# Performance work log

Hardware: AMD Instinct MI355X
Metric: run time of the kernel (lower is better)

The kernel has to match this reference:

```python
import jax, jax.numpy as jnp
import numpy as np

N, M, D = 4096, 4096, 16


def setup_inputs() -> dict:
    key = jax.random.key(0)
    k1, k2, k3, k4 = jax.random.split(key, 4)
    x = jax.random.normal(k1, (N, D), dtype=jnp.float32)
    xx = jax.random.normal(k2, (M, D), dtype=jnp.float32)
    # free-form (pre-softplus) kernel parameters
    scale_ff = jax.random.uniform(k3, (D,), dtype=jnp.float32)
    variance_ff = jax.random.uniform(k4, (), dtype=jnp.float32)
    return {"x": x, "xx": xx, "scale_ff": scale_ff, "variance_ff": variance_ff}


def reference(x, xx, scale_ff, variance_ff):
    # positive() in AutoForce is softplus (free_form is its inverse)
    scale = jax.nn.softplus(scale_ff)          # [D]
    variance = jax.nn.softplus(variance_ff)    # scalar (diag amplitude)
    # r: [N, M, D] pairwise scaled differences (the large broadcast intermediate)
    r = (x[:, None, :] - xx[None, :, :]) / scale
    # K = exp(-||r||^2 / 2) * variance, shape [N, M]
    cov = jnp.exp(-0.5 * jnp.sum(r * r, axis=-1)) * variance
    return cov
```

## Files before the change

kernel.cpp:

```cpp
#include <hip/hip_runtime.h>
#include <math.h>


#define NN 4096
#define MM 4096
#define DD 16

__global__ __launch_bounds__(256, 4)
void rbf_kernel(const float* __restrict__ x, const float* __restrict__ xx,
                const float* __restrict__ scale_ff,
                const float* __restrict__ variance_ff,
                float* __restrict__ out) {
  __shared__ __align__(16) float s_inv[DD];
  __shared__ float s_var;
  __shared__ __align__(16) float s_x[64 * DD];

  const int tid  = threadIdx.x;
  const int lane = tid & 63;
  const int wave = tid >> 6;

  const int i0 = blockIdx.y * 64;
  const int j0 = blockIdx.x * 256;

  if (tid < DD) {
    s_inv[tid] = 1.0f / log1pf(expf(scale_ff[tid]));
  }
  if (tid == DD) {
    s_var = log1pf(expf(variance_ff[0]));
  }
  __syncthreads();

  {
    const int row = tid >> 2;
    const int c   = tid & 3;
    float4 xv = *(const float4*)&x[(i0 + row) * DD + c * 4];
    float4 iv = *(const float4*)&s_inv[c * 4];
    xv.x *= iv.x; xv.y *= iv.y; xv.z *= iv.z; xv.w *= iv.w;
    *(float4*)&s_x[row * DD + c * 4] = xv;
  }

  float4 b[4][4];
  {
    float4 iv[4];
#pragma unroll
    for (int c = 0; c < 4; ++c) iv[c] = *(const float4*)&s_inv[c * 4];
    const int jb = j0 + (lane << 2);
#pragma unroll
    for (int r = 0; r < 4; ++r) {
#pragma unroll
      for (int c = 0; c < 4; ++c) {
        float4 v = *(const float4*)&xx[(jb + r) * DD + c * 4];
        v.x *= iv[c].x; v.y *= iv[c].y; v.z *= iv[c].z; v.w *= iv[c].w;
        b[r][c] = v;
      }
    }
  }

  __syncthreads();

  const float var = s_var;
  const int jb = j0 + (lane << 2);

#pragma unroll
  for (int ii = 0; ii < 16; ++ii) {
    const int li = wave * 16 + ii;
    const float4* a4 = (const float4*)&s_x[li * DD];

    float acc0 = 0.f, acc1 = 0.f, acc2 = 0.f, acc3 = 0.f;
#pragma unroll
    for (int c = 0; c < 4; ++c) {
      const float4 a = a4[c];
      float d;
      d = a.x - b[0][c].x; acc0 = fmaf(d, d, acc0);
      d = a.y - b[0][c].y; acc0 = fmaf(d, d, acc0);
      d = a.z - b[0][c].z; acc0 = fmaf(d, d, acc0);
      d = a.w - b[0][c].w; acc0 = fmaf(d, d, acc0);

      d = a.x - b[1][c].x; acc1 = fmaf(d, d, acc1);
      d = a.y - b[1][c].y; acc1 = fmaf(d, d, acc1);
      d = a.z - b[1][c].z; acc1 = fmaf(d, d, acc1);
      d = a.w - b[1][c].w; acc1 = fmaf(d, d, acc1);

      d = a.x - b[2][c].x; acc2 = fmaf(d, d, acc2);
      d = a.y - b[2][c].y; acc2 = fmaf(d, d, acc2);
      d = a.z - b[2][c].z; acc2 = fmaf(d, d, acc2);
      d = a.w - b[2][c].w; acc2 = fmaf(d, d, acc2);

      d = a.x - b[3][c].x; acc3 = fmaf(d, d, acc3);
      d = a.y - b[3][c].y; acc3 = fmaf(d, d, acc3);
      d = a.z - b[3][c].z; acc3 = fmaf(d, d, acc3);
      d = a.w - b[3][c].w; acc3 = fmaf(d, d, acc3);
    }

    float4 o;
    o.x = __expf(-0.5f * acc0) * var;
    o.y = __expf(-0.5f * acc1) * var;
    o.z = __expf(-0.5f * acc2) * var;
    o.w = __expf(-0.5f * acc3) * var;
    *(float4*)&out[(size_t)(i0 + li) * MM + jb] = o;
  }
}

extern "C" void kernel_launch(void* const* d_in, const int* in_sizes, int n_in,
                              void* d_out, int out_size, void* d_ws, size_t ws_size,
                              hipStream_t stream) {
  const float* x   = (const float*)d_in[0];
  const float* xx  = (const float*)d_in[1];
  const float* sc  = (const float*)d_in[2];
  const float* var = (const float*)d_in[3];
  float* out = (float*)d_out;

  dim3 grid(MM / 256, NN / 64);
  dim3 block(256);
  rbf_kernel<<<grid, block, 0, stream>>>(x, xx, sc, var, out);
}
```

Measured before the change: 93.17 us.

## Expand squared distance into norms plus dot product, fold variance into exponent

Rewrites ||a-b||^2/2 as |a|^2/2 + |b|^2/2 - a·b, with per-row norms precomputed once (x norms in padded shared memory, xx norms in registers). The log of the variance is folded into the exponent, so the inner loop becomes pure FMAs and the per-output multiply disappears. The shared row stride is padded to 20 floats, and the row loop is unrolled by 2 instead of fully. The expansion can lose precision through cancellation for close points, and the kernel is probably bound by output store bandwidth anyway.

```diff
diff --git a/kernel.cpp b/kernel.cpp
--- a/kernel.cpp
+++ b/kernel.cpp
@@ -5,6 +5,7 @@
 #define NN 4096
 #define MM 4096
 #define DD 16
+#define RS 20
 
 __global__ __launch_bounds__(256, 4)
 void rbf_kernel(const float* __restrict__ x, const float* __restrict__ xx,
@@ -12,8 +13,8 @@
                 const float* __restrict__ variance_ff,
                 float* __restrict__ out) {
   __shared__ __align__(16) float s_inv[DD];
-  __shared__ float s_var;
-  __shared__ __align__(16) float s_x[64 * DD];
+  __shared__ float s_lnvar;
+  __shared__ __align__(16) float s_a[64 * RS];
 
   const int tid  = threadIdx.x;
   const int lane = tid & 63;
@@ -26,7 +27,7 @@
     s_inv[tid] = 1.0f / log1pf(expf(scale_ff[tid]));
   }
   if (tid == DD) {
-    s_var = log1pf(expf(variance_ff[0]));
+    s_lnvar = logf(log1pf(expf(variance_ff[0])));
   }
   __syncthreads();
 
@@ -36,10 +37,23 @@
     float4 xv = *(const float4*)&x[(i0 + row) * DD + c * 4];
     float4 iv = *(const float4*)&s_inv[c * 4];
     xv.x *= iv.x; xv.y *= iv.y; xv.z *= iv.z; xv.w *= iv.w;
-    *(float4*)&s_x[row * DD + c * 4] = xv;
+    *(float4*)&s_a[row * RS + c * 4] = xv;
+  }
+  __syncthreads();
+
+  if (tid < 64) {
+    float s = 0.f;
+#pragma unroll
+    for (int c = 0; c < 4; ++c) {
+      float4 v = *(const float4*)&s_a[tid * RS + c * 4];
+      s = fmaf(v.x, v.x, s); s = fmaf(v.y, v.y, s);
+      s = fmaf(v.z, v.z, s); s = fmaf(v.w, v.w, s);
+    }
+    s_a[tid * RS + DD] = 0.5f * s - s_lnvar;
   }
 
   float4 b[4][4];
+  float dn[4];
   {
     float4 iv[4];
 #pragma unroll
@@ -47,56 +61,53 @@
     const int jb = j0 + (lane << 2);
 #pragma unroll
     for (int r = 0; r < 4; ++r) {
+      float s = 0.f;
 #pragma unroll
       for (int c = 0; c < 4; ++c) {
-        float4 v = *(const float4*)&xx[(jb + r) * DD + c * 4];
+        float4 v = *(const float4*)&xx[(size_t)(jb + r) * DD + c * 4];
         v.x *= iv[c].x; v.y *= iv[c].y; v.z *= iv[c].z; v.w *= iv[c].w;
         b[r][c] = v;
+        s = fmaf(v.x, v.x, s); s = fmaf(v.y, v.y, s);
+        s = fmaf(v.z, v.z, s); s = fmaf(v.w, v.w, s);
       }
+      dn[r] = 0.5f * s;
     }
   }
 
   __syncthreads();
 
-  const float var = s_var;
   const int jb = j0 + (lane << 2);
 
-#pragma unroll
+#pragma unroll 2
   for (int ii = 0; ii < 16; ++ii) {
     const int li = wave * 16 + ii;
-    const float4* a4 = (const float4*)&s_x[li * DD];
+    const float* ap = &s_a[li * RS];
+    const float4 a0 = *(const float4*)&ap[0];
+    const float4 a1 = *(const float4*)&ap[4];
+    const float4 a2 = *(const float4*)&ap[8];
+    const float4 a3 = *(const float4*)&ap[12];
+    const float cc  = ap[DD];
 
-    float acc0 = 0.f, acc1 = 0.f, acc2 = 0.f, acc3 = 0.f;
+    float acc[4] = {0.f, 0.f, 0.f, 0.f};
 #pragma unroll
-    for (int c = 0; c < 4; ++c) {
-      const float4 a = a4[c];
-      float d;
-      d = a.x - b[0][c].x; acc0 = fmaf(d, d, acc0);
-      d = a.y - b[0][c].y; acc0 = fmaf(d, d, acc0);
-      d = a.z - b[0][c].z; acc0 = fmaf(d, d, acc0);
-      d = a.w - b[0][c].w; acc0 = fmaf(d, d, acc0);
-
-      d = a.x - b[1][c].x; acc1 = fmaf(d, d, acc1);
-      d = a.y - b[1][c].y; acc1 = fmaf(d, d, acc1);
-      d = a.z - b[1][c].z; acc1 = fmaf(d, d, acc1);
-      d = a.w - b[1][c].w; acc1 = fmaf(d, d, acc1);
-
-      d = a.x - b[2][c].x; acc2 = fmaf(d, d, acc2);
-      d = a.y - b[2][c].y; acc2 = fmaf(d, d, acc2);
-      d = a.z - b[2][c].z; acc2 = fmaf(d, d, acc2);
-      d = a.w - b[2][c].w; acc2 = fmaf(d, d, acc2);
-
-      d = a.x - b[3][c].x; acc3 = fmaf(d, d, acc3);
-      d = a.y - b[3][c].y; acc3 = fmaf(d, d, acc3);
-      d = a.z - b[3][c].z; acc3 = fmaf(d, d, acc3);
-      d = a.w - b[3][c].w; acc3 = fmaf(d, d, acc3);
+    for (int r = 0; r < 4; ++r) {
+      float s = 0.f;
+      s = fmaf(a0.x, b[r][0].x, s); s = fmaf(a0.y, b[r][0].y, s);
+      s = fmaf(a0.z, b[r][0].z, s); s = fmaf(a0.w, b[r][0].w, s);
+      s = fmaf(a1.x, b[r][1].x, s); s = fmaf(a1.y, b[r][1].y, s);
+      s = fmaf(a1.z, b[r][1].z, s); s = fmaf(a1.w, b[r][1].w, s);
+      s = fmaf(a2.x, b[r][2].x, s); s = fmaf(a2.y, b[r][2].y, s);
+      s = fmaf(a2.z, b[r][2].z, s); s = fmaf(a2.w, b[r][2].w, s);
+      s = fmaf(a3.x, b[r][3].x, s); s = fmaf(a3.y, b[r][3].y, s);
+      s = fmaf(a3.z, b[r][3].z, s); s = fmaf(a3.w, b[r][3].w, s);
+      acc[r] = s;
     }
 
     float4 o;
-    o.x = __expf(-0.5f * acc0) * var;
-    o.y = __expf(-0.5f * acc1) * var;
-    o.z = __expf(-0.5f * acc2) * var;
-    o.w = __expf(-0.5f * acc3) * var;
+    o.x = __expf(acc[0] - cc - dn[0]);
+    o.y = __expf(acc[1] - cc - dn[1]);
+    o.z = __expf(acc[2] - cc - dn[2]);
+    o.w = __expf(acc[3] - cc - dn[3]);
     *(float4*)&out[(size_t)(i0 + li) * MM + jb] = o;
   }
 }
```

Result: faster. 90.28 us (-3.1%).
